# Kernel tuning notes

Measured on AMD Instinct MI355X. Metric: run time of the kernel, lower is better.

## Reference

```python
import jax, jax.numpy as jnp
import numpy as np

D_MODEL = 1024
D_STATE = 16  # hardcoded in original: A = randn(d_model, 16)


def setup_inputs() -> dict:
    key = jax.random.key(0)
    ks = jax.random.split(key, 9)
    D = D_MODEL
    s = 1.0 / np.sqrt(D)
    x = jax.random.normal(ks[0], (4, 8192, D), dtype=jnp.float32)
    in_w = jax.random.uniform(ks[1], (2 * D, D), minval=-s, maxval=s, dtype=jnp.float32)
    in_b = jax.random.uniform(ks[2], (2 * D,), minval=-s, maxval=s, dtype=jnp.float32)
    out_w = jax.random.uniform(ks[3], (D, D), minval=-s, maxval=s, dtype=jnp.float32)
    out_b = jax.random.uniform(ks[4], (D,), minval=-s, maxval=s, dtype=jnp.float32)
    dt_w = jax.random.uniform(ks[5], (D, D), minval=-s, maxval=s, dtype=jnp.float32)
    dt_b = jax.random.uniform(ks[6], (D,), minval=-s, maxval=s, dtype=jnp.float32)
    A = jax.random.normal(ks[7], (D, D_STATE), dtype=jnp.float32)
    Dp = jax.random.normal(ks[8], (D,), dtype=jnp.float32)
    return {"x": x, "in_w": in_w, "in_b": in_b, "out_w": out_w, "out_b": out_b,
            "dt_w": dt_w, "dt_b": dt_b, "A": A, "Dp": Dp}


def reference(x, in_w, in_b, out_w, out_b, dt_w, dt_b, A, Dp):
    # x: [B, L, D]. in_proj -> [B, L, 2D], split into x_val / res.
    x_and_res = jnp.einsum('bld,ed->ble', x, in_w) + in_b
    x_val, res = jnp.split(x_and_res, 2, axis=-1)
    # Original computes dt = softplus(dt_proj(xt)) per timestep but never uses it
    # (dead compute, A/Dp/h also unused); output depends only on silu gating.
    # y_t = xt * sigmoid(xt) == silu(x_val), fully parallel over L (no recurrence).
    y = x_val * jax.nn.sigmoid(x_val)
    gated = y * jax.nn.silu(res)
    return jnp.einsum('bld,ed->ble', gated, out_w) + out_b
```

## Files before the change

kernel.cpp:

```cpp
#include <hip/hip_runtime.h>
#include <cstdint>


typedef __bf16 bf16x8 __attribute__((ext_vector_type(8)));
typedef float f32x4 __attribute__((ext_vector_type(4)));

#define M_TOTAL 32768
#define KD 1024

__device__ __forceinline__ void gload_lds16(const void* g, void* lds_u) {
  __builtin_amdgcn_global_load_lds(
      (__attribute__((address_space(1))) void*)(uintptr_t)g,
      (__attribute__((address_space(3))) void*)(uint32_t)(uintptr_t)lds_u,
      16, 0, 0);
}

__device__ __forceinline__ float silu_f(float v) {
  return v / (1.0f + __expf(-v));
}

__global__ void cast_f32_to_bf16_x8(const float* __restrict__ in,
                                    __bf16* __restrict__ out, int n8) {
  int i = blockIdx.x * blockDim.x + threadIdx.x;
  if (i >= n8) return;
  const float4* p = (const float4*)in;
  float4 v0 = p[2 * i];
  float4 v1 = p[2 * i + 1];
  bf16x8 o;
  o[0] = (__bf16)v0.x; o[1] = (__bf16)v0.y; o[2] = (__bf16)v0.z; o[3] = (__bf16)v0.w;
  o[4] = (__bf16)v1.x; o[5] = (__bf16)v1.y; o[6] = (__bf16)v1.z; o[7] = (__bf16)v1.w;
  ((bf16x8*)out)[i] = o;
}

__global__ __launch_bounds__(256, 2)
void gemm1_silu(const __bf16* __restrict__ X, const __bf16* __restrict__ W1,
                const float* __restrict__ in_b, __bf16* __restrict__ G) {
  __shared__ __bf16 lA[128 * 32];
  __shared__ __bf16 lB1[128 * 32];
  __shared__ __bf16 lB2[128 * 32];

  const int t = threadIdx.x;
  const int w = t >> 6;
  const int lane = t & 63;
  const int wr = w >> 1, wc = w & 1;
  const int lr = lane & 15;
  const int lk = lane >> 4;

  const long m0 = (long)blockIdx.y * 128;
  const int n0 = blockIdx.x * 128;

  const int srow = t >> 2;
  const int sblk = t & 3;
  const __bf16* gA = X + (m0 + srow) * KD + sblk * 8;
  const __bf16* gB1 = W1 + (size_t)(n0 + srow) * KD + sblk * 8;
  const __bf16* gB2 = W1 + (size_t)(n0 + 1024 + srow) * KD + sblk * 8;
  __bf16* lAw = lA + w * 512;
  __bf16* lB1w = lB1 + w * 512;
  __bf16* lB2w = lB2 + w * 512;

  f32x4 accX[4][4] = {};
  f32x4 accR[4][4] = {};

  for (int k0 = 0; k0 < KD; k0 += 32) {
    gload_lds16(gA, lAw);
    gload_lds16(gA + 64 * KD, lAw + 2048);
    gload_lds16(gB1, lB1w);
    gload_lds16(gB1 + 64 * KD, lB1w + 2048);
    gload_lds16(gB2, lB2w);
    gload_lds16(gB2 + 64 * KD, lB2w + 2048);
    gA += 32; gB1 += 32; gB2 += 32;
    __syncthreads();

    bf16x8 a[4], b1[4], b2[4];
#pragma unroll
    for (int i = 0; i < 4; ++i)
      a[i] = *(const bf16x8*)(lA + (wr * 64 + i * 16 + lr) * 32 + lk * 8);
#pragma unroll
    for (int j = 0; j < 4; ++j) {
      b1[j] = *(const bf16x8*)(lB1 + (wc * 64 + j * 16 + lr) * 32 + lk * 8);
      b2[j] = *(const bf16x8*)(lB2 + (wc * 64 + j * 16 + lr) * 32 + lk * 8);
    }
#pragma unroll
    for (int i = 0; i < 4; ++i)
#pragma unroll
      for (int j = 0; j < 4; ++j) {
        accX[i][j] = __builtin_amdgcn_mfma_f32_16x16x32_bf16(a[i], b1[j], accX[i][j], 0, 0, 0);
        accR[i][j] = __builtin_amdgcn_mfma_f32_16x16x32_bf16(a[i], b2[j], accR[i][j], 0, 0, 0);
      }
    __syncthreads();
  }

#pragma unroll
  for (int i = 0; i < 4; ++i)
#pragma unroll
    for (int j = 0; j < 4; ++j)
#pragma unroll
      for (int q = 0; q < 4; ++q) {
        const int r = wr * 64 + i * 16 + (lane >> 4) * 4 + q;
        const int c = wc * 64 + j * 16 + (lane & 15);
        const long row = m0 + r;
        const int col = n0 + c;
        float xv = accX[i][j][q] + in_b[col];
        float rs = accR[i][j][q] + in_b[col + 1024];
        G[row * KD + col] = (__bf16)(silu_f(xv) * silu_f(rs));
      }
}

__global__ __launch_bounds__(256, 2)
void gemm2_bias(const __bf16* __restrict__ G, const __bf16* __restrict__ W2,
                const float* __restrict__ out_b, float* __restrict__ OUT) {
  __shared__ __bf16 lA[128 * 32];
  __shared__ __bf16 lB[128 * 32];

  const int t = threadIdx.x;
  const int w = t >> 6;
  const int lane = t & 63;
  const int wr = w >> 1, wc = w & 1;
  const int lr = lane & 15;
  const int lk = lane >> 4;

  const long m0 = (long)blockIdx.y * 128;
  const int n0 = blockIdx.x * 128;

  const int srow = t >> 2;
  const int sblk = t & 3;
  const __bf16* gA = G + (m0 + srow) * KD + sblk * 8;
  const __bf16* gB = W2 + (size_t)(n0 + srow) * KD + sblk * 8;
  __bf16* lAw = lA + w * 512;
  __bf16* lBw = lB + w * 512;

  f32x4 acc[4][4] = {};

  for (int k0 = 0; k0 < KD; k0 += 32) {
    gload_lds16(gA, lAw);
    gload_lds16(gA + 64 * KD, lAw + 2048);
    gload_lds16(gB, lBw);
    gload_lds16(gB + 64 * KD, lBw + 2048);
    gA += 32; gB += 32;
    __syncthreads();

    bf16x8 a[4], b[4];
#pragma unroll
    for (int i = 0; i < 4; ++i)
      a[i] = *(const bf16x8*)(lA + (wr * 64 + i * 16 + lr) * 32 + lk * 8);
#pragma unroll
    for (int j = 0; j < 4; ++j)
      b[j] = *(const bf16x8*)(lB + (wc * 64 + j * 16 + lr) * 32 + lk * 8);
#pragma unroll
    for (int i = 0; i < 4; ++i)
#pragma unroll
      for (int j = 0; j < 4; ++j)
        acc[i][j] = __builtin_amdgcn_mfma_f32_16x16x32_bf16(a[i], b[j], acc[i][j], 0, 0, 0);
    __syncthreads();
  }

#pragma unroll
  for (int i = 0; i < 4; ++i)
#pragma unroll
    for (int j = 0; j < 4; ++j)
#pragma unroll
      for (int q = 0; q < 4; ++q) {
        const int r = wr * 64 + i * 16 + (lane >> 4) * 4 + q;
        const int c = wc * 64 + j * 16 + (lane & 15);
        OUT[(m0 + r) * KD + n0 + c] = acc[i][j][q] + out_b[n0 + c];
      }
}

extern "C" void kernel_launch(void* const* d_in, const int* in_sizes, int n_in,
                              void* d_out, int out_size, void* d_ws, size_t ws_size,
                              hipStream_t stream) {
  const float* x = (const float*)d_in[0];
  const float* in_w = (const float*)d_in[1];
  const float* in_b = (const float*)d_in[2];
  const float* out_w = (const float*)d_in[3];
  const float* out_b = (const float*)d_in[4];

  char* ws = (char*)d_ws;
  __bf16* xb = (__bf16*)(ws);
  __bf16* w1b = (__bf16*)(ws + (size_t)67108864);
  __bf16* w2b = (__bf16*)(ws + (size_t)71303168);
  __bf16* gb = (__bf16*)(ws + (size_t)73400320);

  cast_f32_to_bf16_x8<<<dim3(16384), 256, 0, stream>>>(x, xb, 33554432 / 8);
  cast_f32_to_bf16_x8<<<dim3(1024), 256, 0, stream>>>(in_w, w1b, 2097152 / 8);
  cast_f32_to_bf16_x8<<<dim3(512), 256, 0, stream>>>(out_w, w2b, 1048576 / 8);

  gemm1_silu<<<dim3(8, 256), 256, 0, stream>>>(xb, w1b, in_b, gb);
  gemm2_bias<<<dim3(8, 256), 256, 0, stream>>>(gb, w2b, out_b, (float*)d_out);
}
```

Before: 315.8 us.

## Rewrite GEMMs with 256x256 tiles, triple-buffered LDS pipeline, interleaved W1

Both GEMM kernels are rebuilt around a shared core with 256x256 tiles, 512 threads, a three-stage LDS ring filled by async global-to-LDS loads under vmcnt waits, XOR-swizzled LDS addressing, and MFMA priority raising. The in_proj weight is re-laid out so x and res rows interleave, and gemm1's epilogue pairs them with a lane shuffle. Block indices are swizzled for L2 locality. The goals are hiding load latency, raising arithmetic intensity per LDS byte and avoiding bank conflicts. In exchange register pressure rises and the epilogue's strided bf16 stores may coalesce poorly.

```diff
diff --git a/kernel.cpp b/kernel.cpp
--- a/kernel.cpp
+++ b/kernel.cpp
@@ -5,8 +5,9 @@
 typedef __bf16 bf16x8 __attribute__((ext_vector_type(8)));
 typedef float f32x4 __attribute__((ext_vector_type(4)));
 
-#define M_TOTAL 32768
 #define KD 1024
+#define NT 32
+#define BUF_ELEMS 16384
 
 __device__ __forceinline__ void gload_lds16(const void* g, void* lds_u) {
   __builtin_amdgcn_global_load_lds(
@@ -18,6 +19,10 @@
 __device__ __forceinline__ float silu_f(float v) {
   return v / (1.0f + __expf(-v));
 }
+
+#define WAITB(N) do { \
+  asm volatile("s_waitcnt vmcnt(" #N ")" ::: "memory"); \
+  asm volatile("s_barrier" ::: "memory"); } while (0)
 
 __global__ void cast_f32_to_bf16_x8(const float* __restrict__ in,
                                     __bf16* __restrict__ out, int n8) {
@@ -32,137 +37,166 @@
   ((bf16x8*)out)[i] = o;
 }
 
-__global__ __launch_bounds__(256, 2)
-void gemm1_silu(const __bf16* __restrict__ X, const __bf16* __restrict__ W1,
-                const float* __restrict__ in_b, __bf16* __restrict__ G) {
-  __shared__ __bf16 lA[128 * 32];
-  __shared__ __bf16 lB1[128 * 32];
-  __shared__ __bf16 lB2[128 * 32];
-
+__global__ void cast_w1_interleave(const float* __restrict__ in,
+                                   __bf16* __restrict__ out) {
+  int i = blockIdx.x * blockDim.x + threadIdx.x;
+  int orow = i >> 7;
+  int chunk = i & 127;
+  int srow = (orow >> 1) + ((orow & 1) << 10);
+  const float4* p = (const float4*)(in + ((size_t)srow << 10) + (chunk << 3));
+  float4 v0 = p[0], v1 = p[1];
+  bf16x8 o;
+  o[0] = (__bf16)v0.x; o[1] = (__bf16)v0.y; o[2] = (__bf16)v0.z; o[3] = (__bf16)v0.w;
+  o[4] = (__bf16)v1.x; o[5] = (__bf16)v1.y; o[6] = (__bf16)v1.z; o[7] = (__bf16)v1.w;
+  *(bf16x8*)(out + ((size_t)orow << 10) + (chunk << 3)) = o;
+}
+
+template <int BUF>
+__device__ __forceinline__ void stage_tile(const __bf16*& pa, const __bf16*& pb,
+                                           __bf16* smw) {
+  __bf16* d = smw + BUF * BUF_ELEMS;
+  gload_lds16(pa, d);
+  gload_lds16(pa + 128 * KD, d + 4096);
+  gload_lds16(pb, d + 8192);
+  gload_lds16(pb + 128 * KD, d + 12288);
+  pa += 32;
+  pb += 32;
+}
+
+template <int BUF>
+__device__ __forceinline__ void compute_tile(const __bf16* sm, int aoff, int boff,
+                                             f32x4 (&acc)[8][4]) {
+  const __bf16* base = sm + BUF * BUF_ELEMS;
+  bf16x8 af[8], bf[4];
+#pragma unroll
+  for (int i = 0; i < 8; ++i)
+    af[i] = *(const bf16x8*)(base + aoff + i * 512);
+#pragma unroll
+  for (int j = 0; j < 4; ++j)
+    bf[j] = *(const bf16x8*)(base + boff + j * 512);
+  __builtin_amdgcn_s_setprio(1);
+#pragma unroll
+  for (int i = 0; i < 8; ++i)
+#pragma unroll
+    for (int j = 0; j < 4; ++j)
+      acc[i][j] = __builtin_amdgcn_mfma_f32_16x16x32_bf16(af[i], bf[j], acc[i][j], 0, 0, 0);
+  __builtin_amdgcn_s_setprio(0);
+}
+
+__device__ __forceinline__ void gemm_core(const __bf16* __restrict__ A,
+                                          const __bf16* __restrict__ B,
+                                          __bf16* sm, long m0, long n0,
+                                          f32x4 (&acc)[8][4]) {
   const int t = threadIdx.x;
   const int w = t >> 6;
   const int lane = t & 63;
-  const int wr = w >> 1, wc = w & 1;
   const int lr = lane & 15;
   const int lk = lane >> 4;
-
-  const long m0 = (long)blockIdx.y * 128;
-  const int n0 = blockIdx.x * 128;
-
-  const int srow = t >> 2;
-  const int sblk = t & 3;
-  const __bf16* gA = X + (m0 + srow) * KD + sblk * 8;
-  const __bf16* gB1 = W1 + (size_t)(n0 + srow) * KD + sblk * 8;
-  const __bf16* gB2 = W1 + (size_t)(n0 + 1024 + srow) * KD + sblk * 8;
-  __bf16* lAw = lA + w * 512;
-  __bf16* lB1w = lB1 + w * 512;
-  __bf16* lB2w = lB2 + w * 512;
-
-  f32x4 accX[4][4] = {};
-  f32x4 accR[4][4] = {};
-
-  for (int k0 = 0; k0 < KD; k0 += 32) {
-    gload_lds16(gA, lAw);
-    gload_lds16(gA + 64 * KD, lAw + 2048);
-    gload_lds16(gB1, lB1w);
-    gload_lds16(gB1 + 64 * KD, lB1w + 2048);
-    gload_lds16(gB2, lB2w);
-    gload_lds16(gB2 + 64 * KD, lB2w + 2048);
-    gA += 32; gB1 += 32; gB2 += 32;
-    __syncthreads();
-
-    bf16x8 a[4], b1[4], b2[4];
-#pragma unroll
-    for (int i = 0; i < 4; ++i)
-      a[i] = *(const bf16x8*)(lA + (wr * 64 + i * 16 + lr) * 32 + lk * 8);
-#pragma unroll
-    for (int j = 0; j < 4; ++j) {
-      b1[j] = *(const bf16x8*)(lB1 + (wc * 64 + j * 16 + lr) * 32 + lk * 8);
-      b2[j] = *(const bf16x8*)(lB2 + (wc * 64 + j * 16 + lr) * 32 + lk * 8);
-    }
-#pragma unroll
-    for (int i = 0; i < 4; ++i)
-#pragma unroll
-      for (int j = 0; j < 4; ++j) {
-        accX[i][j] = __builtin_amdgcn_mfma_f32_16x16x32_bf16(a[i], b1[j], accX[i][j], 0, 0, 0);
-        accR[i][j] = __builtin_amdgcn_mfma_f32_16x16x32_bf16(a[i], b2[j], accR[i][j], 0, 0, 0);
+  const int wr = w >> 2;
+  const int wc = w & 3;
+
+  const int l = lane;
+  const int stg_row = w * 16 + (l >> 2);
+  const int stg_col = ((l & 3) ^ ((l >> 3) & 3)) << 3;
+  const __bf16* pa = A + (m0 + stg_row) * KD + stg_col;
+  const __bf16* pb = B + (n0 + stg_row) * KD + stg_col;
+  __bf16* smw = sm + w * 512;
+
+  const int swz8 = (lk ^ ((lr >> 1) & 3)) << 3;
+  const int aoff = (wr * 128 + lr) * 32 + swz8;
+  const int boff = 8192 + (wc * 64 + lr) * 32 + swz8;
+
+#pragma unroll
+  for (int i = 0; i < 8; ++i)
+#pragma unroll
+    for (int j = 0; j < 4; ++j)
+      acc[i][j] = (f32x4){0.f, 0.f, 0.f, 0.f};
+
+  stage_tile<0>(pa, pb, smw);
+  stage_tile<1>(pa, pb, smw);
+
+  for (int it = 0; it < 10; ++it) {
+    WAITB(4); stage_tile<2>(pa, pb, smw); compute_tile<0>(sm, aoff, boff, acc);
+    WAITB(4); stage_tile<0>(pa, pb, smw); compute_tile<1>(sm, aoff, boff, acc);
+    WAITB(4); stage_tile<1>(pa, pb, smw); compute_tile<2>(sm, aoff, boff, acc);
+  }
+  WAITB(4); compute_tile<0>(sm, aoff, boff, acc);
+  WAITB(0); compute_tile<1>(sm, aoff, boff, acc);
+}
+
+__global__ __launch_bounds__(512, 2)
+void gemm1_silu(const __bf16* __restrict__ X, const __bf16* __restrict__ W1i,
+                const float* __restrict__ in_b, __bf16* __restrict__ G) {
+  __shared__ __bf16 sm[3 * BUF_ELEMS];
+  const int bid = blockIdx.x;
+  const int swz = (bid & 7) * 128 + (bid >> 3);
+  const int m_idx = swz >> 3;
+  const int n_idx = swz & 7;
+  const long m0 = (long)m_idx * 256;
+  const long n0 = (long)n_idx * 256;
+
+  f32x4 acc[8][4];
+  gemm_core(X, W1i, sm, m0, n0, acc);
+
+  const int lane = threadIdx.x & 63;
+  const int w = threadIdx.x >> 6;
+  const int wr = w >> 2, wc = w & 3;
+
+  float bj[4];
+#pragma unroll
+  for (int j = 0; j < 4; ++j) {
+    int nn = (int)n0 + wc * 64 + j * 16 + (lane & 15);
+    bj[j] = (nn & 1) ? in_b[1024 + (nn >> 1)] : in_b[nn >> 1];
+  }
+#pragma unroll
+  for (int i = 0; i < 8; ++i)
+#pragma unroll
+    for (int j = 0; j < 4; ++j)
+#pragma unroll
+      for (int q = 0; q < 4; ++q) {
+        int r = wr * 128 + i * 16 + (lane >> 4) * 4 + q;
+        float v = acc[i][j][q] + bj[j];
+        float s = silu_f(v);
+        float p = __shfl_xor(s, 1);
+        float g = s * p;
+        if (!(lane & 1)) {
+          int nn = (int)n0 + wc * 64 + j * 16 + (lane & 15);
+          G[(m0 + r) * 1024 + (nn >> 1)] = (__bf16)g;
+        }
       }
-    __syncthreads();
-  }
-
-#pragma unroll
-  for (int i = 0; i < 4; ++i)
-#pragma unroll
-    for (int j = 0; j < 4; ++j)
-#pragma unroll
-      for (int q = 0; q < 4; ++q) {
-        const int r = wr * 64 + i * 16 + (lane >> 4) * 4 + q;
-        const int c = wc * 64 + j * 16 + (lane & 15);
-        const long row = m0 + r;
-        const int col = n0 + c;
-        float xv = accX[i][j][q] + in_b[col];
-        float rs = accR[i][j][q] + in_b[col + 1024];
-        G[row * KD + col] = (__bf16)(silu_f(xv) * silu_f(rs));
-      }
-}
-
-__global__ __launch_bounds__(256, 2)
+}
+
+__global__ __launch_bounds__(512, 2)
 void gemm2_bias(const __bf16* __restrict__ G, const __bf16* __restrict__ W2,
                 const float* __restrict__ out_b, float* __restrict__ OUT) {
-  __shared__ __bf16 lA[128 * 32];
-  __shared__ __bf16 lB[128 * 32];
-
-  const int t = threadIdx.x;
-  const int w = t >> 6;
-  const int lane = t & 63;
-  const int wr = w >> 1, wc = w & 1;
-  const int lr = lane & 15;
-  const int lk = lane >> 4;
-
-  const long m0 = (long)blockIdx.y * 128;
-  const int n0 = blockIdx.x * 128;
-
-  const int srow = t >> 2;
-  const int sblk = t & 3;
-  const __bf16* gA = G + (m0 + srow) * KD + sblk * 8;
-  const __bf16* gB = W2 + (size_t)(n0 + srow) * KD + sblk * 8;
-  __bf16* lAw = lA + w * 512;
-  __bf16* lBw = lB + w * 512;
-
-  f32x4 acc[4][4] = {};
-
-  for (int k0 = 0; k0 < KD; k0 += 32) {
-    gload_lds16(gA, lAw);
-    gload_lds16(gA + 64 * KD, lAw + 2048);
-    gload_lds16(gB, lBw);
-    gload_lds16(gB + 64 * KD, lBw + 2048);
-    gA += 32; gB += 32;
-    __syncthreads();
-
-    bf16x8 a[4], b[4];
-#pragma unroll
-    for (int i = 0; i < 4; ++i)
-      a[i] = *(const bf16x8*)(lA + (wr * 64 + i * 16 + lr) * 32 + lk * 8);
-#pragma unroll
-    for (int j = 0; j < 4; ++j)
-      b[j] = *(const bf16x8*)(lB + (wc * 64 + j * 16 + lr) * 32 + lk * 8);
-#pragma unroll
-    for (int i = 0; i < 4; ++i)
-#pragma unroll
-      for (int j = 0; j < 4; ++j)
-        acc[i][j] = __builtin_amdgcn_mfma_f32_16x16x32_bf16(a[i], b[j], acc[i][j], 0, 0, 0);
-    __syncthreads();
-  }
-
-#pragma unroll
-  for (int i = 0; i < 4; ++i)
+  __shared__ __bf16 sm[3 * BUF_ELEMS];
+  const int bid = blockIdx.x;
+  const int swz = (bid & 7) * 64 + (bid >> 3);
+  const int m_idx = swz >> 2;
+  const int n_idx = swz & 3;
+  const long m0 = (long)m_idx * 256;
+  const long n0 = (long)n_idx * 256;
+
+  f32x4 acc[8][4];
+  gemm_core(G, W2, sm, m0, n0, acc);
+
+  const int lane = threadIdx.x & 63;
+  const int w = threadIdx.x >> 6;
+  const int wr = w >> 2, wc = w & 3;
+
+  float ob[4];
+#pragma unroll
+  for (int j = 0; j < 4; ++j)
+    ob[j] = out_b[(int)n0 + wc * 64 + j * 16 + (lane & 15)];
+#pragma unroll
+  for (int i = 0; i < 8; ++i)
 #pragma unroll
     for (int j = 0; j < 4; ++j)
 #pragma unroll
       for (int q = 0; q < 4; ++q) {
-        const int r = wr * 64 + i * 16 + (lane >> 4) * 4 + q;
-        const int c = wc * 64 + j * 16 + (lane & 15);
-        OUT[(m0 + r) * KD + n0 + c] = acc[i][j][q] + out_b[n0 + c];
+        int r = wr * 128 + i * 16 + (lane >> 4) * 4 + q;
+        int c = wc * 64 + j * 16 + (lane & 15);
+        OUT[(m0 + r) * 1024 + n0 + c] = acc[i][j][q] + ob[j];
       }
 }
 
@@ -182,9 +216,9 @@
   __bf16* gb = (__bf16*)(ws + (size_t)73400320);
 
   cast_f32_to_bf16_x8<<<dim3(16384), 256, 0, stream>>>(x, xb, 33554432 / 8);
-  cast_f32_to_bf16_x8<<<dim3(1024), 256, 0, stream>>>(in_w, w1b, 2097152 / 8);
+  cast_w1_interleave<<<dim3(1024), 256, 0, stream>>>(in_w, w1b);
   cast_f32_to_bf16_x8<<<dim3(512), 256, 0, stream>>>(out_w, w2b, 1048576 / 8);
 
-  gemm1_silu<<<dim3(8, 256), 256, 0, stream>>>(xb, w1b, in_b, gb);
-  gemm2_bias<<<dim3(8, 256), 256, 0, stream>>>(gb, w2b, out_b, (float*)d_out);
-}
+  gemm1_silu<<<dim3(1024), 512, 0, stream>>>(xb, w1b, in_b, gb);
+  gemm2_bias<<<dim3(512), 512, 0, stream>>>(gb, w2b, out_b, (float*)d_out);
+}
```

Result: faster. 291.7 us (-7.6%).
